# Performance work log

Hardware: AMD Instinct MI355X
Metric: run time of the kernel (lower is better)

The kernel has to match this reference:

```python
import jax, jax.numpy as jnp
import numpy as np

B, T, E, H, R = 1, 2048, 4096, 16, 64
D = E // H
SCALE_ATTN = float(np.sqrt(D))


def _i8_linear(x, W, b, alpha, beta):
    # W8A8B8O8Linear: int8 in, int8 weight/bias, int8 out with requant epilogue
    acc = jnp.einsum('bte,oe->bto', x.astype(jnp.int32), W.astype(jnp.int32)).astype(jnp.float32)
    y = alpha * acc + beta * b.astype(jnp.float32)
    return jnp.clip(jnp.round(y), -128, 127).astype(jnp.int8)


def _rotate_every_two(x):
    x1, x2 = x[..., ::2], x[..., 1::2]
    return jnp.stack([-x2, x1], axis=-1).reshape(x.shape)


def _sincos(seq_len, dim):
    inv_freq = 1.0 / (10000.0 ** (jnp.arange(0, dim, 2, dtype=jnp.float32) / dim))
    ang = jnp.arange(seq_len, dtype=jnp.float32)[:, None] * inv_freq[None, :]
    return jnp.sin(ang), jnp.cos(ang)


def _apply_rotary(x, sin, cos):
    # duplicate_interleave -> repeat each freq twice along last dim
    sin = jnp.repeat(sin, 2, axis=-1)[None, :, None, :]
    cos = jnp.repeat(cos, 2, axis=-1)[None, :, None, :]
    return x * cos + _rotate_every_two(x) * sin


def setup_inputs():
    key = jax.random.key(0)
    ks = jax.random.split(key, 9)
    i8 = lambda k, s: jax.random.randint(k, s, -128, 128, dtype=jnp.int32).astype(jnp.int8)
    return {
        'hidden_states': i8(ks[0], (B, T, E)),
        'Wq': i8(ks[1], (E, E)), 'bq': i8(ks[2], (E,)),
        'Wk': i8(ks[3], (E, E)), 'bk': i8(ks[4], (E,)),
        'Wv': i8(ks[5], (E, E)), 'bv': i8(ks[6], (E,)),
        'Wo': i8(ks[7], (E, E)),
        'b_out': jax.random.normal(ks[8], (E,), dtype=jnp.float32),
        'alpha_q': 2e-4, 'beta_q': 1.0,
        'alpha_k': 2e-4, 'beta_k': 1.0,
        'alpha_v': 2e-4, 'beta_v': 1.0,
        'alpha_qk': 1e-3, 'alpha_pv': 1e-2, 'alpha_out': 2e-4,
    }


def reference(hidden_states, Wq, bq, Wk, bk, Wv, bv, Wo, b_out,
              alpha_q, beta_q, alpha_k, beta_k, alpha_v, beta_v,
              alpha_qk, alpha_pv, alpha_out):
    # int8 q/k/v projections -> [B, T, H, D]
    q = _i8_linear(hidden_states, Wq, bq, alpha_q, beta_q).reshape(B, T, H, D)
    k = _i8_linear(hidden_states, Wk, bk, alpha_k, beta_k).reshape(B, T, H, D)
    v = _i8_linear(hidden_states, Wv, bv, alpha_v, beta_v).reshape(B, T, H, D)
    v = v.transpose(0, 2, 1, 3)  # [B, H, T, D] int8

    # fused rotary on first R dims (float math on dequantized-per-tensor int8 codes)
    sin, cos = _sincos(T, R)
    qf, kf = q.astype(jnp.float32), k.astype(jnp.float32)
    qf = jnp.concatenate([_apply_rotary(qf[..., :R], sin, cos), qf[..., R:]], axis=-1)
    kf = jnp.concatenate([_apply_rotary(kf[..., :R], sin, cos), kf[..., R:]], axis=-1)
    # torch .to(int8) truncates toward zero
    to_i8 = lambda x: jnp.clip(jnp.trunc(x), -128, 127).astype(jnp.int8)
    q = to_i8(qf.transpose(0, 2, 1, 3))  # [B, H, T, D]
    k = to_i8(kf.transpose(0, 2, 1, 3))

    scores = alpha_qk * jnp.einsum('bhtd,bhsd->bhts', q.astype(jnp.int32), k.astype(jnp.int32)).astype(jnp.float32)
    causal = jnp.tril(jnp.ones((T, T), dtype=bool))
    scores = jnp.where(causal, scores, jnp.finfo(jnp.float32).min)
    probs = jax.nn.softmax(scores / SCALE_ATTN, axis=-1)
    probs = jnp.round(probs * 127.0).astype(jnp.int8)  # requant probs to int8

    acc = jnp.einsum('bhts,bhsd->bhtd', probs.astype(jnp.int32), v.astype(jnp.int32)).astype(jnp.float32)
    attn_out = jnp.clip(jnp.round(alpha_pv * acc), -128, 127).astype(jnp.int8)
    attn_out = attn_out.transpose(0, 2, 1, 3).reshape(B, T, E)  # merge heads

    # W8A8BFP32OFP32Linear
    out = alpha_out * jnp.einsum('bte,oe->bto', attn_out.astype(jnp.int32), Wo.astype(jnp.int32)).astype(jnp.float32) + b_out
    return out
```

## Files before the change

kernel.cpp:

```cpp
#include <hip/hip_runtime.h>
#include <cstdint>
#include <cmath>

#define T_ 2048
#define E_ 4096
#define H_ 16
#define D_ 256
#define NF 32

typedef int v4i  __attribute__((ext_vector_type(4)));

__device__ __forceinline__ int dot4(int a, int b, int c) {
#if __has_builtin(__builtin_amdgcn_sdot4)
  return __builtin_amdgcn_sdot4(a, b, c, false);
#else
  c += ((a << 24) >> 24) * ((b << 24) >> 24);
  c += ((a << 16) >> 24) * ((b << 16) >> 24);
  c += ((a <<  8) >> 24) * ((b <<  8) >> 24);
  c += (a >> 24) * (b >> 24);
  return c;
#endif
}

__device__ __forceinline__ int pack4i(int4 v) {
  return (v.x & 255) | ((v.y & 255) << 8) | ((v.z & 255) << 16) | (v.w << 24);
}

#define GLD_LDS16(g, l)                                                        \
  __builtin_amdgcn_global_load_lds(                                            \
      (const __attribute__((address_space(1))) void*)(g),                      \
      (__attribute__((address_space(3))) void*)(l), 16, 0, 0)

__global__ void sincos_kernel(float* __restrict__ sinT, float* __restrict__ cosT) {
  int idx = blockIdx.x * 256 + threadIdx.x;
  int t = idx >> 5, j = idx & 31;
  float invf = (float)exp(-(double)j * (log(10000.0) / 32.0));
  float ang = (float)t * invf;
  sinT[idx] = (float)sin((double)ang);
  cosT[idx] = (float)cos((double)ang);
}

__global__ __launch_bounds__(256) void repack5_kernel(
    const int* __restrict__ sx, const int* __restrict__ s1,
    const int* __restrict__ s2, const int* __restrict__ s3,
    const int* __restrict__ s4,
    int8_t* __restrict__ dx, int8_t* __restrict__ d1,
    int8_t* __restrict__ d2, int8_t* __restrict__ d3,
    int8_t* __restrict__ d4) {
  const int w = blockIdx.y;
  if (w == 0 && blockIdx.x >= (T_ * E_ / 16) / 256) return;
  const int* __restrict__ src =
      (w == 0) ? sx : (w == 1 ? s1 : (w == 2 ? s2 : (w == 3 ? s3 : s4)));
  int8_t* __restrict__ dst =
      (w == 0) ? dx : (w == 1 ? d1 : (w == 2 ? d2 : (w == 3 ? d3 : d4)));
  size_t i = (size_t)blockIdx.x * 256 + threadIdx.x;
  const int4* s = (const int4*)src + i * 4;
  int4 a = s[0], b = s[1], c = s[2], d = s[3];
  int4 o;
  o.x = pack4i(a); o.y = pack4i(b); o.z = pack4i(c); o.w = pack4i(d);
  ((int4*)dst)[i] = o;
}

__global__ __launch_bounds__(256, 2) void qkv_fused_mfma(
    const int8_t* __restrict__ x8,
    const int8_t* __restrict__ Wq8, const int* __restrict__ bq,
    const int8_t* __restrict__ Wk8, const int* __restrict__ bk,
    const int8_t* __restrict__ Wv8, const int* __restrict__ bv,
    const float* __restrict__ alpq, const float* __restrict__ betq,
    const float* __restrict__ alpk, const float* __restrict__ betk,
    const float* __restrict__ alpv, const float* __restrict__ betv,
    const float* __restrict__ sinT, const float* __restrict__ cosT,
    int8_t* __restrict__ Q8, int8_t* __restrict__ K8, int8_t* __restrict__ VT)
{
  __shared__ int8_t As[2][8192];
  __shared__ int8_t Bs[2][3][8192];

  const int tid  = threadIdx.x;
  const int wave = tid >> 6, lane = tid & 63;
  const int wm = wave >> 1, wn = wave & 1;
  const int t0 = blockIdx.x * 128, o0 = blockIdx.y * 128;

  const int srow = lane >> 2;
  const int scol = ((lane & 3) ^ ((lane >> 3) & 3)) * 16;
  const int col  = lane & 15;
  const int quad = lane >> 4;

  v4i accQ[4][4] = {}, accK[4][4] = {}, accV[4][4] = {};

  const int8_t* gA0 = x8  + (size_t)(t0 + wave * 32 + srow) * E_ + scol;
  const int8_t* gBq = Wq8 + (size_t)(o0 + wave * 32 + srow) * E_ + scol;
  const int8_t* gBk = Wk8 + (size_t)(o0 + wave * 32 + srow) * E_ + scol;
  const int8_t* gBv = Wv8 + (size_t)(o0 + wave * 32 + srow) * E_ + scol;

#define STAGE_F(bufi, kt) do {                                                 \
    const int e0_ = (kt) * 64;                                                 \
    GLD_LDS16(gA0 + e0_,           As[bufi] + wave * 2048);                    \
    GLD_LDS16(gA0 + e0_ + 16 * E_, As[bufi] + wave * 2048 + 1024);             \
    GLD_LDS16(gBq + e0_,           Bs[bufi][0] + wave * 2048);                 \
    GLD_LDS16(gBq + e0_ + 16 * E_, Bs[bufi][0] + wave * 2048 + 1024);          \
    GLD_LDS16(gBk + e0_,           Bs[bufi][1] + wave * 2048);                 \
    GLD_LDS16(gBk + e0_ + 16 * E_, Bs[bufi][1] + wave * 2048 + 1024);          \
    GLD_LDS16(gBv + e0_,           Bs[bufi][2] + wave * 2048);                 \
    GLD_LDS16(gBv + e0_ + 16 * E_, Bs[bufi][2] + wave * 2048 + 1024);          \
  } while (0)

  int aoff[4], boff[4];
  #pragma unroll
  for (int i = 0; i < 4; ++i) {
    const int ra = wm * 64 + i * 16 + col;
    aoff[i] = ra * 64 + ((quad ^ ((ra >> 1) & 3)) * 16);
    const int rb = wn * 64 + i * 16 + col;
    boff[i] = rb * 64 + ((quad ^ ((rb >> 1) & 3)) * 16);
  }

  STAGE_F(0, 0);
  STAGE_F(1, 1);

  for (int kt = 0; kt < 64; ++kt) {
    const int cur = kt & 1;
    if (kt == 63) asm volatile("s_waitcnt vmcnt(0)" ::: "memory");
    else          asm volatile("s_waitcnt vmcnt(8)" ::: "memory");
    __builtin_amdgcn_s_barrier();
    v4i a[4];
    #pragma unroll
    for (int i = 0; i < 4; ++i)
      a[i] = *(const v4i*)(As[cur] + aoff[i]);
    __builtin_amdgcn_s_setprio(1);
    {
      v4i b[4];
      #pragma unroll
      for (int j = 0; j < 4; ++j) b[j] = *(const v4i*)(Bs[cur][0] + boff[j]);
      #pragma unroll
      for (int i = 0; i < 4; ++i)
        #pragma unroll
        for (int j = 0; j < 4; ++j)
          accQ[i][j] = __builtin_amdgcn_mfma_i32_16x16x64_i8(a[i], b[j], accQ[i][j], 0, 0, 0);
      #pragma unroll
      for (int j = 0; j < 4; ++j) b[j] = *(const v4i*)(Bs[cur][1] + boff[j]);
      #pragma unroll
      for (int i = 0; i < 4; ++i)
        #pragma unroll
        for (int j = 0; j < 4; ++j)
          accK[i][j] = __builtin_amdgcn_mfma_i32_16x16x64_i8(a[i], b[j], accK[i][j], 0, 0, 0);
      #pragma unroll
      for (int j = 0; j < 4; ++j) b[j] = *(const v4i*)(Bs[cur][2] + boff[j]);
      #pragma unroll
      for (int i = 0; i < 4; ++i)
        #pragma unroll
        for (int j = 0; j < 4; ++j)
          accV[i][j] = __builtin_amdgcn_mfma_i32_16x16x64_i8(a[i], b[j], accV[i][j], 0, 0, 0);
    }
    __builtin_amdgcn_s_setprio(0);
    __builtin_amdgcn_s_barrier();
    if (kt + 2 < 64) STAGE_F(cur, kt + 2);
  }
#undef STAGE_F

  const bool ropeWave = ((o0 & 128) == 0) && (wn == 0);
  #pragma unroll
  for (int m = 0; m < 3; ++m) {
    const int* __restrict__ bsp = (m == 0) ? bq : (m == 1 ? bk : bv);
    const float alpha = (m == 0) ? alpq[0] : (m == 1 ? alpk[0] : alpv[0]);
    const float beta  = (m == 0) ? betq[0] : (m == 1 ? betk[0] : betv[0]);
    int8_t* __restrict__ dst = (m == 0) ? Q8 : (m == 1 ? K8 : VT);
    #pragma unroll
    for (int j = 0; j < 4; ++j) {
      const int o  = o0 + wn * 64 + j * 16 + col;
      const int h  = o >> 8;
      const int dd = o & 255;
      const float bb = (float)bsp[o];
      const int jj = dd >> 1;
      #pragma unroll
      for (int i = 0; i < 4; ++i) {
        const int tb = t0 + wm * 64 + i * 16 + quad * 4;
        int qb[4];
        #pragma unroll
        for (int r = 0; r < 4; ++r) {
          float v = __fadd_rn(__fmul_rn(alpha, (float)(m == 0 ? accQ[i][j][r]
                                         : (m == 1 ? accK[i][j][r] : accV[i][j][r]))),
                              __fmul_rn(beta, bb));
          v = rintf(v);
          v = fminf(fmaxf(v, -128.0f), 127.0f);
          qb[r] = (int)v;
        }
        if (m < 2 && ropeWave) {
          #pragma unroll
          for (int r = 0; r < 4; ++r) {
            float y  = (float)qb[r];
            float yo = __shfl_xor(y, 1);
            const int t = tb + r;
            const float s = sinT[t * NF + jj];
            const float c = cosT[t * NF + jj];
            float rv = ((col & 1) == 0)
                ? __fadd_rn(__fmul_rn(y, c), __fmul_rn(-yo, s))
                : __fadd_rn(__fmul_rn(y, c), __fmul_rn(yo, s));
            qb[r] = (int)fminf(fmaxf(truncf(rv), -128.0f), 127.0f);
          }
        }
        if (m == 2) {
          int packed = (qb[0] & 255) | ((qb[1] & 255) << 8) |
                       ((qb[2] & 255) << 16) | ((qb[3] & 255) << 24);
          *(int*)(dst + ((size_t)h * 256 + dd) * T_ + tb) = packed;
        } else {
          #pragma unroll
          for (int r = 0; r < 4; ++r)
            dst[((size_t)h * T_ + tb + r) * D_ + dd] = (int8_t)qb[r];
        }
      }
    }
  }
}

__global__ __launch_bounds__(256, 3) void out_gemm_mfma(
    const int8_t* __restrict__ xa, const int8_t* __restrict__ Wo8,
    const float* __restrict__ b_out, const float* __restrict__ p_aout,
    float* __restrict__ out)
{
  const float alpha = p_aout[0];
  __shared__ int8_t As[3][8192];
  __shared__ int8_t Bs[3][8192];

  const int tid  = threadIdx.x;
  const int wave = tid >> 6, lane = tid & 63;
  const int wm = wave >> 1, wn = wave & 1;
  const int t0 = blockIdx.x * 128, o0 = blockIdx.y * 128;
  const int srow = lane >> 2;
  const int scol = ((lane & 3) ^ ((lane >> 3) & 3)) * 16;
  const int col = lane & 15, quad = lane >> 4;

  v4i acc[4][4] = {};
  const int8_t* gA0 = xa  + (size_t)(t0 + wave * 32 + srow) * E_ + scol;
  const int8_t* gB0 = Wo8 + (size_t)(o0 + wave * 32 + srow) * E_ + scol;

#define STAGE_OUT(bufi, kt) do {                                               \
    const int e0_ = (kt) * 64;                                                 \
    GLD_LDS16(gA0 + e0_,           As[bufi] + wave * 2048);                    \
    GLD_LDS16(gA0 + e0_ + 16 * E_, As[bufi] + wave * 2048 + 1024);             \
    GLD_LDS16(gB0 + e0_,           Bs[bufi] + wave * 2048);                    \
    GLD_LDS16(gB0 + e0_ + 16 * E_, Bs[bufi] + wave * 2048 + 1024);             \
  } while (0)

  int aoff[4], boff[4];
  #pragma unroll
  for (int i = 0; i < 4; ++i) {
    const int ra = wm * 64 + i * 16 + col;
    aoff[i] = ra * 64 + ((quad ^ ((ra >> 1) & 3)) * 16);
    const int rb = wn * 64 + i * 16 + col;
    boff[i] = rb * 64 + ((quad ^ ((rb >> 1) & 3)) * 16);
  }

  STAGE_OUT(0, 0);
  STAGE_OUT(1, 1);

  int cur = 0;
  for (int kt = 0; kt < 64; ++kt) {
    if (kt == 63) asm volatile("s_waitcnt vmcnt(0)" ::: "memory");
    else          asm volatile("s_waitcnt vmcnt(4)" ::: "memory");
    __builtin_amdgcn_s_barrier();
    if (kt < 62) {
      int nb = cur + 2; if (nb >= 3) nb -= 3;
      STAGE_OUT(nb, kt + 2);
    }
    v4i a[4], b[4];
    #pragma unroll
    for (int i = 0; i < 4; ++i)
      a[i] = *(const v4i*)(As[cur] + aoff[i]);
    #pragma unroll
    for (int j = 0; j < 4; ++j)
      b[j] = *(const v4i*)(Bs[cur] + boff[j]);
    __builtin_amdgcn_s_setprio(1);
    #pragma unroll
    for (int i = 0; i < 4; ++i)
      #pragma unroll
      for (int j = 0; j < 4; ++j)
        acc[i][j] = __builtin_amdgcn_mfma_i32_16x16x64_i8(a[i], b[j], acc[i][j], 0, 0, 0);
    __builtin_amdgcn_s_setprio(0);
    cur = (cur == 2) ? 0 : cur + 1;
  }
#undef STAGE_OUT

  #pragma unroll
  for (int j = 0; j < 4; ++j) {
    const int o = o0 + wn * 64 + j * 16 + col;
    const float bb = b_out[o];
    #pragma unroll
    for (int i = 0; i < 4; ++i) {
      #pragma unroll
      for (int r = 0; r < 4; ++r) {
        const int t = t0 + wm * 64 + i * 16 + quad * 4 + r;
        out[(size_t)t * E_ + o] = __fadd_rn(__fmul_rn(alpha, (float)acc[i][j][r]), bb);
      }
    }
  }
}

__global__ __launch_bounds__(256) void attn_ms_chunk(
    const int8_t* __restrict__ Q8, const int8_t* __restrict__ K8,
    const float* __restrict__ p_aqk,
    float* __restrict__ mPart, float* __restrict__ sPart)
{
  const int ch = blockIdx.x;
  const int qi = blockIdx.y;
  const int h  = blockIdx.z;
  if ((ch << 2) > qi) return;

  __shared__ int8_t Qs[4 * 4096];
  __shared__ int8_t KVs[16384];
  __shared__ float  mred[64][2];
  __shared__ float  sred[64][2];

  const int t0  = qi * 64;
  const int tid = threadIdx.x;
  const int wave = tid >> 6, lane = tid & 63;
  const int wm = wave >> 1, wn = wave & 1;
  const int col = lane & 15, quad = lane >> 4;
  const int srow = lane >> 2, scol = (lane & 3) * 16;
  const float aqk = p_aqk[0] * 0.0625f;

  {
    const int8_t* g = Q8 + ((size_t)h * T_ + t0 + wave * 16 + srow) * D_ + scol;
    #pragma unroll
    for (int c = 0; c < 4; ++c)
      GLD_LDS16(g + c * 64, Qs + c * 4096 + wave * 1024);
  }

  const int it0 = ch * 4;
  const int it1 = (it0 + 3 < qi) ? (it0 + 3) : qi;

  float m[8], sm[8];
  #pragma unroll
  for (int u = 0; u < 8; ++u) { m[u] = -INFINITY; sm[u] = 0.0f; }

  for (int it = it0; it <= it1; ++it) {
    const int s0 = it * 64;
    __syncthreads();
    {
      const int8_t* g = K8 + ((size_t)h * T_ + s0 + wave * 16 + srow) * D_ + scol;
      #pragma unroll
      for (int c = 0; c < 4; ++c)
        GLD_LDS16(g + c * 64, KVs + c * 4096 + wave * 1024);
    }
    __syncthreads();
    v4i accS[2][2] = {};
    #pragma unroll
    for (int c = 0; c < 4; ++c) {
      v4i a[2], b[2];
      #pragma unroll
      for (int i = 0; i < 2; ++i)
        a[i] = *(const v4i*)(Qs + c * 4096 + (wm * 32 + i * 16 + col) * 64 + quad * 16);
      #pragma unroll
      for (int j = 0; j < 2; ++j)
        b[j] = *(const v4i*)(KVs + c * 4096 + (wn * 32 + j * 16 + col) * 64 + quad * 16);
      #pragma unroll
      for (int i = 0; i < 2; ++i)
        #pragma unroll
        for (int j = 0; j < 2; ++j)
          accS[i][j] = __builtin_amdgcn_mfma_i32_16x16x64_i8(a[i], b[j], accS[i][j], 0, 0, 0);
    }
    const bool diag = (s0 == t0);
    #pragma unroll
    for (int i = 0; i < 2; ++i) {
      #pragma unroll
      for (int r = 0; r < 4; ++r) {
        const int ri = i * 4 + r;
        const int qrow = t0 + wm * 32 + i * 16 + quad * 4 + r;
        #pragma unroll
        for (int j = 0; j < 2; ++j) {
          const int s = s0 + wn * 32 + j * 16 + col;
          if (!diag || s <= qrow) {
            float l = __fmul_rn(aqk, (float)accS[i][j][r]);
            if (l > m[ri]) { sm[ri] = sm[ri] * expf(m[ri] - l) + 1.0f; m[ri] = l; }
            else           { sm[ri] += expf(l - m[ri]); }
          }
        }
      }
    }
  }

  #pragma unroll
  for (int u = 0; u < 8; ++u) {
    #pragma unroll
    for (int off = 1; off < 16; off <<= 1) {
      float om = __shfl_xor(m[u], off);
      float os = __shfl_xor(sm[u], off);
      float mm = fmaxf(m[u], om);
      float e1 = (m[u] == mm) ? 1.0f : expf(m[u] - mm);
      float e2 = (om   == mm) ? 1.0f : expf(om - mm);
      sm[u] = sm[u] * e1 + os * e2;
      m[u] = mm;
    }
  }
  __syncthreads();
  if (col == 0) {
    #pragma unroll
    for (int u = 0; u < 8; ++u) {
      int row = wm * 32 + (u >> 2) * 16 + quad * 4 + (u & 3);
      mred[row][wn] = m[u];
      sred[row][wn] = sm[u];
    }
  }
  __syncthreads();
  if (col == 0 && wn == 0) {
    #pragma unroll
    for (int u = 0; u < 8; ++u) {
      int row = wm * 32 + (u >> 2) * 16 + quad * 4 + (u & 3);
      float m0 = mred[row][0], m1 = mred[row][1];
      float sa = sred[row][0], sb = sred[row][1];
      float mm = fmaxf(m0, m1);
      float e0 = (m0 == mm) ? 1.0f : expf(m0 - mm);
      float e1 = (m1 == mm) ? 1.0f : expf(m1 - mm);
      size_t base = (((size_t)h * 32 + qi) * 64 + row) * 8 + ch;
      mPart[base] = mm;
      sPart[base] = __fadd_rn(__fmul_rn(sa, e0), __fmul_rn(sb, e1));
    }
  }
}

__global__ __launch_bounds__(256) void attn_pv_chunk(
    const int8_t* __restrict__ Q8, const int8_t* __restrict__ K8,
    const int8_t* __restrict__ VT,
    const float* __restrict__ p_aqk,
    const float* __restrict__ mPart, const float* __restrict__ sPart,
    int* __restrict__ P0, int* __restrict__ P1)
{
  const int cc = blockIdx.x;
  const int qi = 31 - blockIdx.y;
  const int h  = blockIdx.z;
  if (cc == 1 && qi < 16) return;

  __shared__ int8_t Qs[4 * 4096];
  __shared__ int8_t KVs[16384];
  __shared__ int8_t Ps[64][64];

  const int t0  = qi * 64;
  const int tid = threadIdx.x;
  const int wave = tid >> 6, lane = tid & 63;
  const int wm = wave >> 1, wn = wave & 1;
  const int col = lane & 15, quad = lane >> 4;
  const int srow = lane >> 2, scol = (lane & 3) * 16;
  const float aqk = p_aqk[0] * 0.0625f;

  {
    const int8_t* g = Q8 + ((size_t)h * T_ + t0 + wave * 16 + srow) * D_ + scol;
    #pragma unroll
    for (int c = 0; c < 4; ++c)
      GLD_LDS16(g + c * 64, Qs + c * 4096 + wave * 1024);
  }

  float mF[8], sF[8];
  const int nch = (qi >> 2) + 1;
  #pragma unroll
  for (int u = 0; u < 8; ++u) {
    const int row = wm * 32 + (u >> 2) * 16 + quad * 4 + (u & 3);
    const float* mp = mPart + (((size_t)h * 32 + qi) * 64 + row) * 8;
    const float* sp = sPart + (((size_t)h * 32 + qi) * 64 + row) * 8;
    float m = mp[0], s = sp[0];
    for (int c = 1; c < nch; ++c) {
      float mc = mp[c], sc = sp[c];
      float mm = fmaxf(m, mc);
      float e1 = (m  == mm) ? 1.0f : expf(m - mm);
      float e2 = (mc == mm) ? 1.0f : expf(mc - mm);
      s = __fadd_rn(__fmul_rn(s, e1), __fmul_rn(sc, e2));
      m = mm;
    }
    mF[u] = m;
    sF[u] = s;
  }

  const int it0 = cc * 16;
  const int it1 = (it0 + 15 < qi) ? (it0 + 15) : qi;

  v4i pv[2][8] = {};
  for (int it = it0; it <= it1; ++it) {
    const int s0 = it * 64;
    __syncthreads();
    {
      const int8_t* g = K8 + ((size_t)h * T_ + s0 + wave * 16 + srow) * D_ + scol;
      #pragma unroll
      for (int c = 0; c < 4; ++c)
        GLD_LDS16(g + c * 64, KVs + c * 4096 + wave * 1024);
    }
    __syncthreads();
    v4i accS[2][2] = {};
    #pragma unroll
    for (int c = 0; c < 4; ++c) {
      v4i a[2], b[2];
      #pragma unroll
      for (int i = 0; i < 2; ++i)
        a[i] = *(const v4i*)(Qs + c * 4096 + (wm * 32 + i * 16 + col) * 64 + quad * 16);
      #pragma unroll
      for (int j = 0; j < 2; ++j)
        b[j] = *(const v4i*)(KVs + c * 4096 + (wn * 32 + j * 16 + col) * 64 + quad * 16);
      #pragma unroll
      for (int i = 0; i < 2; ++i)
        #pragma unroll
        for (int j = 0; j < 2; ++j)
          accS[i][j] = __builtin_amdgcn_mfma_i32_16x16x64_i8(a[i], b[j], accS[i][j], 0, 0, 0);
    }
    __syncthreads();
    {
      #pragma unroll
      for (int c = 0; c < 4; ++c) {
        const int drow = (wave * 4 + c) * 16 + srow;
        GLD_LDS16(VT + ((size_t)h * 256 + drow) * T_ + s0 + scol,
                  KVs + (wave * 4 + c) * 1024);
      }
    }
    const bool diag = (s0 == t0);
    #pragma unroll
    for (int i = 0; i < 2; ++i) {
      #pragma unroll
      for (int r = 0; r < 4; ++r) {
        const int ri = i * 4 + r;
        const int qrow = t0 + wm * 32 + i * 16 + quad * 4 + r;
        #pragma unroll
        for (int j = 0; j < 2; ++j) {
          const int s = s0 + wn * 32 + j * 16 + col;
          int q = 0;
          if (!diag || s <= qrow) {
            float l = __fmul_rn(aqk, (float)accS[i][j][r]);
            float p = expf(l - mF[ri]) / sF[ri];
            q = (int)rintf(__fmul_rn(p, 127.0f));
          }
          Ps[wm * 32 + i * 16 + quad * 4 + r][wn * 32 + j * 16 + col] = (int8_t)q;
        }
      }
    }
    __syncthreads();
    v4i a2[2], b2[8];
    #pragma unroll
    for (int i = 0; i < 2; ++i)
      a2[i] = *(const v4i*)&Ps[wm * 32 + i * 16 + col][quad * 16];
    #pragma unroll
    for (int dt = 0; dt < 8; ++dt)
      b2[dt] = *(const v4i*)(KVs + (wn * 128 + dt * 16 + col) * 64 + quad * 16);
    #pragma unroll
    for (int i = 0; i < 2; ++i)
      #pragma unroll
      for (int dt = 0; dt < 8; ++dt)
        pv[i][dt] = __builtin_amdgcn_mfma_i32_16x16x64_i8(a2[i], b2[dt], pv[i][dt], 0, 0, 0);
  }

  int* __restrict__ dst = (cc == 0)
      ? P0 + (((size_t)h * 32 + qi) << 14)
      : P1 + (((size_t)h * 16 + (qi - 16)) << 14);
  #pragma unroll
  for (int i = 0; i < 2; ++i) {
    #pragma unroll
    for (int r = 0; r < 4; ++r) {
      const int trow = wm * 32 + i * 16 + quad * 4 + r;
      #pragma unroll
      for (int dt = 0; dt < 8; ++dt) {
        const int d = wn * 128 + dt * 16 + col;
        dst[trow * 256 + d] = pv[i][dt][r];
      }
    }
  }
}

__global__ __launch_bounds__(256) void attn_pv_combine(
    const int* __restrict__ P0, const int* __restrict__ P1,
    const float* __restrict__ p_apv, int8_t* __restrict__ attn8)
{
  const float apv = p_apv[0];
  int idx = blockIdx.x * 256 + threadIdx.x;
  int d4  = idx & 63;
  int row = (idx >> 6) & 63;
  int qi  = (idx >> 12) & 31;
  int h   = idx >> 17;
  size_t off = (((size_t)h * 32 + qi) << 14) + row * 256 + d4 * 4;
  int4 a = *(const int4*)(P0 + off);
  if (qi >= 16) {
    size_t off1 = (((size_t)h * 16 + (qi - 16)) << 14) + row * 256 + d4 * 4;
    int4 b1 = *(const int4*)(P1 + off1);
    a.x += b1.x; a.y += b1.y; a.z += b1.z; a.w += b1.w;
  }
  int q[4];
  int vv[4] = {a.x, a.y, a.z, a.w};
  #pragma unroll
  for (int r = 0; r < 4; ++r) {
    float y = rintf(__fmul_rn(apv, (float)vv[r]));
    y = fminf(fmaxf(y, -128.0f), 127.0f);
    q[r] = (int)y;
  }
  int packed = (q[0] & 255) | ((q[1] & 255) << 8) | ((q[2] & 255) << 16) | ((q[3] & 255) << 24);
  int t = qi * 64 + row;
  *(int*)(attn8 + (size_t)t * E_ + h * D_ + d4 * 4) = packed;
}

__global__ __launch_bounds__(256) void attn_mfma(
    const int8_t* __restrict__ Q8, const int8_t* __restrict__ K8,
    const int8_t* __restrict__ VT,
    const float* __restrict__ p_aqk, const float* __restrict__ p_apv,
    int8_t* __restrict__ attn8)
{
  __shared__ int8_t Qs[4 * 4096];
  __shared__ int8_t KVs[16384];
  __shared__ int8_t Ps[64][64];
  __shared__ float  mred[64][2];
  __shared__ float  sred[64][2];

  const int h   = blockIdx.y;
  const int t0  = blockIdx.x * 64;
  const int tid = threadIdx.x;
  const int wave = tid >> 6, lane = tid & 63;
  const int wm = wave >> 1, wn = wave & 1;
  const int col = lane & 15, quad = lane >> 4;
  const int srow = lane >> 2, scol = (lane & 3) * 16;
  const float aqk = p_aqk[0] * 0.0625f;
  const float apv = p_apv[0];

  {
    const int8_t* g = Q8 + ((size_t)h * T_ + t0 + wave * 16 + srow) * D_ + scol;
    #pragma unroll
    for (int c = 0; c < 4; ++c)
      GLD_LDS16(g + c * 64, Qs + c * 4096 + wave * 1024);
  }

  const int nt = t0 / 64 + 1;

  float m[8], sm[8];
  #pragma unroll
  for (int u = 0; u < 8; ++u) { m[u] = -INFINITY; sm[u] = 0.0f; }

  for (int it = 0; it < nt; ++it) {
    const int s0 = it * 64;
    __syncthreads();
    {
      const int8_t* g = K8 + ((size_t)h * T_ + s0 + wave * 16 + srow) * D_ + scol;
      #pragma unroll
      for (int c = 0; c < 4; ++c)
        GLD_LDS16(g + c * 64, KVs + c * 4096 + wave * 1024);
    }
    __syncthreads();
    v4i accS[2][2] = {};
    #pragma unroll
    for (int c = 0; c < 4; ++c) {
      v4i a[2], b[2];
      #pragma unroll
      for (int i = 0; i < 2; ++i)
        a[i] = *(const v4i*)(Qs + c * 4096 + (wm * 32 + i * 16 + col) * 64 + quad * 16);
      #pragma unroll
      for (int j = 0; j < 2; ++j)
        b[j] = *(const v4i*)(KVs + c * 4096 + (wn * 32 + j * 16 + col) * 64 + quad * 16);
      #pragma unroll
      for (int i = 0; i < 2; ++i)
        #pragma unroll
        for (int j = 0; j < 2; ++j)
          accS[i][j] = __builtin_amdgcn_mfma_i32_16x16x64_i8(a[i], b[j], accS[i][j], 0, 0, 0);
    }
    const bool diag = (s0 == t0);
    #pragma unroll
    for (int i = 0; i < 2; ++i) {
      #pragma unroll
      for (int r = 0; r < 4; ++r) {
        const int ri = i * 4 + r;
        const int qrow = t0 + wm * 32 + i * 16 + quad * 4 + r;
        #pragma unroll
        for (int j = 0; j < 2; ++j) {
          const int s = s0 + wn * 32 + j * 16 + col;
          if (!diag || s <= qrow) {
            float l = __fmul_rn(aqk, (float)accS[i][j][r]);
            if (l > m[ri]) { sm[ri] = sm[ri] * expf(m[ri] - l) + 1.0f; m[ri] = l; }
            else           { sm[ri] += expf(l - m[ri]); }
          }
        }
      }
    }
  }

  #pragma unroll
  for (int u = 0; u < 8; ++u) {
    #pragma unroll
    for (int off = 1; off < 16; off <<= 1) {
      float om = __shfl_xor(m[u], off);
      float os = __shfl_xor(sm[u], off);
      float mm = fmaxf(m[u], om);
      float e1 = (m[u] == mm) ? 1.0f : expf(m[u] - mm);
      float e2 = (om   == mm) ? 1.0f : expf(om - mm);
      sm[u] = sm[u] * e1 + os * e2;
      m[u] = mm;
    }
  }
  __syncthreads();
  if (col == 0) {
    #pragma unroll
    for (int u = 0; u < 8; ++u) {
      int row = wm * 32 + (u >> 2) * 16 + quad * 4 + (u & 3);
      mred[row][wn] = m[u];
      sred[row][wn] = sm[u];
    }
  }
  __syncthreads();
  float mF[8], sF[8];
  #pragma unroll
  for (int u = 0; u < 8; ++u) {
    int row = wm * 32 + (u >> 2) * 16 + quad * 4 + (u & 3);
    float m0 = mred[row][0], m1 = mred[row][1];
    float sa = sred[row][0], sb = sred[row][1];
    float mm = fmaxf(m0, m1);
    float e0 = (m0 == mm) ? 1.0f : expf(m0 - mm);
    float e1 = (m1 == mm) ? 1.0f : expf(m1 - mm);
    mF[u] = mm;
    sF[u] = __fadd_rn(__fmul_rn(sa, e0), __fmul_rn(sb, e1));
  }

  v4i pv[2][8] = {};
  for (int it = 0; it < nt; ++it) {
    const int s0 = it * 64;
    __syncthreads();
    {
      const int8_t* g = K8 + ((size_t)h * T_ + s0 + wave * 16 + srow) * D_ + scol;
      #pragma unroll
      for (int c = 0; c < 4; ++c)
        GLD_LDS16(g + c * 64, KVs + c * 4096 + wave * 1024);
    }
    __syncthreads();
    v4i accS[2][2] = {};
    #pragma unroll
    for (int c = 0; c < 4; ++c) {
      v4i a[2], b[2];
      #pragma unroll
      for (int i = 0; i < 2; ++i)
        a[i] = *(const v4i*)(Qs + c * 4096 + (wm * 32 + i * 16 + col) * 64 + quad * 16);
      #pragma unroll
      for (int j = 0; j < 2; ++j)
        b[j] = *(const v4i*)(KVs + c * 4096 + (wn * 32 + j * 16 + col) * 64 + quad * 16);
      #pragma unroll
      for (int i = 0; i < 2; ++i)
        #pragma unroll
        for (int j = 0; j < 2; ++j)
          accS[i][j] = __builtin_amdgcn_mfma_i32_16x16x64_i8(a[i], b[j], accS[i][j], 0, 0, 0);
    }
    __syncthreads();
    {
      #pragma unroll
      for (int c = 0; c < 4; ++c) {
        const int drow = (wave * 4 + c) * 16 + srow;
        GLD_LDS16(VT + ((size_t)h * 256 + drow) * T_ + s0 + scol,
                  KVs + (wave * 4 + c) * 1024);
      }
    }
    const bool diag = (s0 == t0);
    #pragma unroll
    for (int i = 0; i < 2; ++i) {
      #pragma unroll
      for (int r = 0; r < 4; ++r) {
        const int ri = i * 4 + r;
        const int qrow = t0 + wm * 32 + i * 16 + quad * 4 + r;
        #pragma unroll
        for (int j = 0; j < 2; ++j) {
          const int s = s0 + wn * 32 + j * 16 + col;
          int q = 0;
          if (!diag || s <= qrow) {
            float l = __fmul_rn(aqk, (float)accS[i][j][r]);
            float p = expf(l - mF[ri]) / sF[ri];
            q = (int)rintf(__fmul_rn(p, 127.0f));
          }
          Ps[wm * 32 + i * 16 + quad * 4 + r][wn * 32 + j * 16 + col] = (int8_t)q;
        }
      }
    }
    __syncthreads();
    v4i a2[2], b2[8];
    #pragma unroll
    for (int i = 0; i < 2; ++i)
      a2[i] = *(const v4i*)&Ps[wm * 32 + i * 16 + col][quad * 16];
    #pragma unroll
    for (int dt = 0; dt < 8; ++dt)
      b2[dt] = *(const v4i*)(KVs + (wn * 128 + dt * 16 + col) * 64 + quad * 16);
    #pragma unroll
    for (int i = 0; i < 2; ++i)
      #pragma unroll
      for (int dt = 0; dt < 8; ++dt)
        pv[i][dt] = __builtin_amdgcn_mfma_i32_16x16x64_i8(a2[i], b2[dt], pv[i][dt], 0, 0, 0);
  }

  #pragma unroll
  for (int i = 0; i < 2; ++i) {
    #pragma unroll
    for (int r = 0; r < 4; ++r) {
      const int t = t0 + wm * 32 + i * 16 + quad * 4 + r;
      #pragma unroll
      for (int dt = 0; dt < 8; ++dt) {
        const int d = wn * 128 + dt * 16 + col;
        float y = rintf(__fmul_rn(apv, (float)pv[i][dt][r]));
        y = fminf(fmaxf(y, -128.0f), 127.0f);
        attn8[(size_t)t * E_ + h * D_ + d] = (int8_t)(int)y;
      }
    }
  }
}

__global__ __launch_bounds__(256) void qkv_gemm_fb(
    const int* __restrict__ xp,
    const int* __restrict__ Wqp, const int* __restrict__ bq,
    const int* __restrict__ Wkp, const int* __restrict__ bk,
    const int* __restrict__ Wvp, const int* __restrict__ bv,
    const float* __restrict__ alpq, const float* __restrict__ betq,
    const float* __restrict__ alpk, const float* __restrict__ betk,
    const float* __restrict__ alpv, const float* __restrict__ betv,
    const float* __restrict__ sinT, const float* __restrict__ cosT,
    int8_t* __restrict__ Q8, int8_t* __restrict__ K8, int8_t* __restrict__ VT)
{
  const int mode = blockIdx.z;
  const int* __restrict__ Wp = (mode == 0) ? Wqp : (mode == 1 ? Wkp : Wvp);
  const int* __restrict__ bs = (mode == 0) ? bq  : (mode == 1 ? bk  : bv);
  const float alpha = (mode == 0) ? alpq[0] : (mode == 1 ? alpk[0] : alpv[0]);
  const float beta  = (mode == 0) ? betq[0] : (mode == 1 ? betk[0] : betv[0]);

  __shared__ int As[64 * 17];
  __shared__ int Bs[64 * 17];
  const int tid = threadIdx.x;
  const int tx = tid & 15, ty = tid >> 4;
  const int t0 = blockIdx.x * 64, o0 = blockIdx.y * 64;
  const int lrow = tid >> 2, lc = tid & 3;
  int acc[4][4] = {};

  for (int e0 = 0; e0 < E_; e0 += 64) {
    const int* xr = xp + (size_t)(t0 + lrow) * E_ + e0 + lc * 16;
    const int* wr = Wp + (size_t)(o0 + lrow) * E_ + e0 + lc * 16;
    int a4[4], b4[4];
    #pragma unroll
    for (int u = 0; u < 4; ++u) a4[u] = pack4i(((const int4*)xr)[u]);
    #pragma unroll
    for (int u = 0; u < 4; ++u) b4[u] = pack4i(((const int4*)wr)[u]);
    __syncthreads();
    int* ap = &As[lrow * 17 + lc * 4];
    ap[0] = a4[0]; ap[1] = a4[1]; ap[2] = a4[2]; ap[3] = a4[3];
    int* bp = &Bs[lrow * 17 + lc * 4];
    bp[0] = b4[0]; bp[1] = b4[1]; bp[2] = b4[2]; bp[3] = b4[3];
    __syncthreads();
    #pragma unroll
    for (int kk = 0; kk < 16; ++kk) {
      int a[4], b[4];
      #pragma unroll
      for (int i = 0; i < 4; ++i) a[i] = As[(ty * 4 + i) * 17 + kk];
      #pragma unroll
      for (int j = 0; j < 4; ++j) b[j] = Bs[(tx * 4 + j) * 17 + kk];
      #pragma unroll
      for (int i = 0; i < 4; ++i)
        #pragma unroll
        for (int j = 0; j < 4; ++j)
          acc[i][j] = dot4(a[i], b[j], acc[i][j]);
    }
  }

  const int ob = o0 + tx * 4;
  const int h  = ob >> 8;
  const int dd = ob & 255;
  #pragma unroll
  for (int i = 0; i < 4; ++i) {
    const int t = t0 + ty * 4 + i;
    float y[4];
    #pragma unroll
    for (int j = 0; j < 4; ++j) {
      float v = __fadd_rn(__fmul_rn(alpha, (float)acc[i][j]),
                          __fmul_rn(beta, (float)bs[ob + j]));
      v = rintf(v);
      y[j] = fminf(fmaxf(v, -128.0f), 127.0f);
    }
    int q0, q1, q2, q3;
    if (mode < 2 && dd < 64) {
      const int j0 = dd >> 1;
      const float s0 = sinT[t * NF + j0],     c0 = cosT[t * NF + j0];
      const float s1 = sinT[t * NF + j0 + 1], c1 = cosT[t * NF + j0 + 1];
      float r0 = __fadd_rn(__fmul_rn(y[0], c0), __fmul_rn(-y[1], s0));
      float r1 = __fadd_rn(__fmul_rn(y[1], c0), __fmul_rn( y[0], s0));
      float r2 = __fadd_rn(__fmul_rn(y[2], c1), __fmul_rn(-y[3], s1));
      float r3 = __fadd_rn(__fmul_rn(y[3], c1), __fmul_rn( y[2], s1));
      q0 = (int)fminf(fmaxf(truncf(r0), -128.0f), 127.0f);
      q1 = (int)fminf(fmaxf(truncf(r1), -128.0f), 127.0f);
      q2 = (int)fminf(fmaxf(truncf(r2), -128.0f), 127.0f);
      q3 = (int)fminf(fmaxf(truncf(r3), -128.0f), 127.0f);
    } else {
      q0 = (int)y[0]; q1 = (int)y[1]; q2 = (int)y[2]; q3 = (int)y[3];
    }
    if (mode == 2) {
      VT[((size_t)h * 256 + dd + 0) * T_ + t] = (int8_t)q0;
      VT[((size_t)h * 256 + dd + 1) * T_ + t] = (int8_t)q1;
      VT[((size_t)h * 256 + dd + 2) * T_ + t] = (int8_t)q2;
      VT[((size_t)h * 256 + dd + 3) * T_ + t] = (int8_t)q3;
    } else {
      int8_t* dst = (mode == 0) ? Q8 : K8;
      int packed = (q0 & 255) | ((q1 & 255) << 8) | ((q2 & 255) << 16) | ((q3 & 255) << 24);
      *(int*)(dst + ((size_t)h * T_ + t) * D_ + dd) = packed;
    }
  }
}

__global__ __launch_bounds__(256) void out_gemm_fb(
    const int8_t* __restrict__ xa, const int* __restrict__ Wop,
    const float* __restrict__ b_out, const float* __restrict__ p_aout,
    float* __restrict__ out)
{
  __shared__ int As[64 * 17];
  __shared__ int Bs[64 * 17];
  const float alpha = p_aout[0];
  const int tid = threadIdx.x;
  const int tx = tid & 15, ty = tid >> 4;
  const int t0 = blockIdx.x * 64, o0 = blockIdx.y * 64;
  const int lrow = tid >> 2, lc = tid & 3;
  int acc[4][4] = {};

  for (int e0 = 0; e0 < E_; e0 += 64) {
    int4 av4 = *(const int4*)(xa + (size_t)(t0 + lrow) * E_ + e0 + lc * 16);
    const int* wr = Wop + (size_t)(o0 + lrow) * E_ + e0 + lc * 16;
    int b4[4];
    #pragma unroll
    for (int u = 0; u < 4; ++u) b4[u] = pack4i(((const int4*)wr)[u]);
    __syncthreads();
    int* ap = &As[lrow * 17 + lc * 4];
    ap[0] = av4.x; ap[1] = av4.y; ap[2] = av4.z; ap[3] = av4.w;
    int* bp = &Bs[lrow * 17 + lc * 4];
    bp[0] = b4[0]; bp[1] = b4[1]; bp[2] = b4[2]; bp[3] = b4[3];
    __syncthreads();
    #pragma unroll
    for (int kk = 0; kk < 16; ++kk) {
      int a[4], b[4];
      #pragma unroll
      for (int i = 0; i < 4; ++i) a[i] = As[(ty * 4 + i) * 17 + kk];
      #pragma unroll
      for (int j = 0; j < 4; ++j) b[j] = Bs[(tx * 4 + j) * 17 + kk];
      #pragma unroll
      for (int i = 0; i < 4; ++i)
        #pragma unroll
        for (int j = 0; j < 4; ++j)
          acc[i][j] = dot4(a[i], b[j], acc[i][j]);
    }
  }
  #pragma unroll
  for (int i = 0; i < 4; ++i) {
    const int t = t0 + ty * 4 + i;
    const int ob = o0 + tx * 4;
    #pragma unroll
    for (int j = 0; j < 4; ++j) {
      out[(size_t)t * E_ + ob + j] =
          __fadd_rn(__fmul_rn(alpha, (float)acc[i][j]), b_out[ob + j]);
    }
  }
}

extern "C" void kernel_launch(void* const* d_in, const int* in_sizes, int n_in,
                              void* d_out, int out_size, void* d_ws, size_t ws_size,
                              hipStream_t stream) {
  const int* hs   = (const int*)d_in[0];
  const int* Wq   = (const int*)d_in[1];
  const int* bq   = (const int*)d_in[2];
  const int* Wk   = (const int*)d_in[3];
  const int* bk   = (const int*)d_in[4];
  const int* Wv   = (const int*)d_in[5];
  const int* bv   = (const int*)d_in[6];
  const int* Wo   = (const int*)d_in[7];
  const float* b_out = (const float*)d_in[8];
  const float* aq   = (const float*)d_in[9];
  const float* btq  = (const float*)d_in[10];
  const float* ak   = (const float*)d_in[11];
  const float* btk  = (const float*)d_in[12];
  const float* av   = (const float*)d_in[13];
  const float* btv  = (const float*)d_in[14];
  const float* aqk  = (const float*)d_in[15];
  const float* apv  = (const float*)d_in[16];
  const float* aout = (const float*)d_in[17];

  const size_t SEG = (size_t)H_ * T_ * D_;
  char* ws = (char*)d_ws;
  int8_t* Q8    = (int8_t*)ws;
  int8_t* K8    = Q8 + SEG;
  int8_t* VT    = K8 + SEG;
  int8_t* attn8 = VT + SEG;
  int8_t* x8    = attn8;
  float*  sinT  = (float*)(ws + 4 * SEG);
  float*  cosT  = sinT + T_ * NF;
  int8_t* Wq8   = (int8_t*)(cosT + T_ * NF);
  int8_t* Wk8   = Wq8 + (size_t)E_ * E_;
  int8_t* Wv8   = Wk8 + (size_t)E_ * E_;
  int8_t* Wo8   = Wv8 + (size_t)E_ * E_;
  const size_t NEED = 4 * SEG + 2 * (size_t)T_ * NF * 4 + 4 * (size_t)E_ * E_;
  const bool big = (ws_size >= NEED);

  sincos_kernel<<<(T_ * NF) / 256, 256, 0, stream>>>(sinT, cosT);

  if (big) {
    repack5_kernel<<<dim3((E_ * E_ / 16) / 256, 5), 256, 0, stream>>>(
        hs, Wq, Wk, Wv, Wo, x8, Wq8, Wk8, Wv8, Wo8);
    qkv_fused_mfma<<<dim3(T_ / 128, E_ / 128), 256, 0, stream>>>(
        x8, Wq8, bq, Wk8, bk, Wv8, bv, aq, btq, ak, btk, av, btv,
        sinT, cosT, Q8, K8, VT);

    int*   P1g   = (int*)Wq8;
    int*   P0g   = (int*)Wk8;
    float* mPart = (float*)attn8;
    float* sPart = mPart + (size_t)H_ * 32 * 64 * 8;

    attn_ms_chunk<<<dim3(8, 32, H_), 256, 0, stream>>>(Q8, K8, aqk, mPart, sPart);
    attn_pv_chunk<<<dim3(2, 32, H_), 256, 0, stream>>>(
        Q8, K8, VT, aqk, mPart, sPart, P0g, P1g);
    attn_pv_combine<<<(H_ * 32 * 64 * 64) / 256, 256, 0, stream>>>(
        P0g, P1g, apv, attn8);

    out_gemm_mfma<<<dim3(T_ / 128, E_ / 128), 256, 0, stream>>>(
        attn8, Wo8, b_out, aout, (float*)d_out);
  } else {
    qkv_gemm_fb<<<dim3(T_ / 64, E_ / 64, 3), 256, 0, stream>>>(
        hs, Wq, bq, Wk, bk, Wv, bv, aq, btq, ak, btk, av, btv,
        sinT, cosT, Q8, K8, VT);
    attn_mfma<<<dim3(T_ / 64, H_), 256, 0, stream>>>(Q8, K8, VT, aqk, apv, attn8);
    out_gemm_fb<<<dim3(T_ / 64, E_ / 64), 256, 0, stream>>>(
        attn8, Wo, b_out, aout, (float*)d_out);
  }
}
```

Before: 704.6 us.

## Split QKV GEMM per projection with triple buffering; prefetch K tiles in attention

The fused QKV kernel, which held three 64-register accumulator sets, becomes one GEMM per projection selected by blockIdx.z. It uses a 3-stage LDS ring that issues the next load right after a single barrier, and launch bounds are raised to 3 blocks per CU. The attention kernels now double-buffer K tiles in LDS with swizzled offsets, and PV reads V operands straight from global memory into registers instead of staging them through LDS. The aim is higher occupancy and overlap of memory with MFMA, at the cost of re-reading x from memory three times and relying on uncoalesced direct V loads.

```diff
diff --git a/kernel.cpp b/kernel.cpp
--- a/kernel.cpp
+++ b/kernel.cpp
@@ -61,7 +61,7 @@
   ((int4*)dst)[i] = o;
 }
 
-__global__ __launch_bounds__(256, 2) void qkv_fused_mfma(
+__global__ __launch_bounds__(256, 3) void qkv_gemm_mfma(
     const int8_t* __restrict__ x8,
     const int8_t* __restrict__ Wq8, const int* __restrict__ bq,
     const int8_t* __restrict__ Wk8, const int* __restrict__ bk,
@@ -72,8 +72,14 @@
     const float* __restrict__ sinT, const float* __restrict__ cosT,
     int8_t* __restrict__ Q8, int8_t* __restrict__ K8, int8_t* __restrict__ VT)
 {
-  __shared__ int8_t As[2][8192];
-  __shared__ int8_t Bs[2][3][8192];
+  const int mode = blockIdx.z;
+  const int8_t* __restrict__ W = (mode == 0) ? Wq8 : (mode == 1 ? Wk8 : Wv8);
+  const int* __restrict__ bs   = (mode == 0) ? bq  : (mode == 1 ? bk  : bv);
+  const float alpha = (mode == 0) ? alpq[0] : (mode == 1 ? alpk[0] : alpv[0]);
+  const float beta  = (mode == 0) ? betq[0] : (mode == 1 ? betk[0] : betv[0]);
+
+  __shared__ int8_t As[3][8192];
+  __shared__ int8_t Bs[3][8192];
 
   const int tid  = threadIdx.x;
   const int wave = tid >> 6, lane = tid & 63;
@@ -85,23 +91,17 @@
   const int col  = lane & 15;
   const int quad = lane >> 4;
 
-  v4i accQ[4][4] = {}, accK[4][4] = {}, accV[4][4] = {};
-
-  const int8_t* gA0 = x8  + (size_t)(t0 + wave * 32 + srow) * E_ + scol;
-  const int8_t* gBq = Wq8 + (size_t)(o0 + wave * 32 + srow) * E_ + scol;
-  const int8_t* gBk = Wk8 + (size_t)(o0 + wave * 32 + srow) * E_ + scol;
-  const int8_t* gBv = Wv8 + (size_t)(o0 + wave * 32 + srow) * E_ + scol;
-
-#define STAGE_F(bufi, kt) do {                                                 \
+  v4i acc[4][4] = {};
+
+  const int8_t* gA0 = x8 + (size_t)(t0 + wave * 32 + srow) * E_ + scol;
+  const int8_t* gB0 = W  + (size_t)(o0 + wave * 32 + srow) * E_ + scol;
+
+#define STAGE_QKV(bufi, kt) do {                                               \
     const int e0_ = (kt) * 64;                                                 \
     GLD_LDS16(gA0 + e0_,           As[bufi] + wave * 2048);                    \
     GLD_LDS16(gA0 + e0_ + 16 * E_, As[bufi] + wave * 2048 + 1024);             \
-    GLD_LDS16(gBq + e0_,           Bs[bufi][0] + wave * 2048);                 \
-    GLD_LDS16(gBq + e0_ + 16 * E_, Bs[bufi][0] + wave * 2048 + 1024);          \
-    GLD_LDS16(gBk + e0_,           Bs[bufi][1] + wave * 2048);                 \
-    GLD_LDS16(gBk + e0_ + 16 * E_, Bs[bufi][1] + wave * 2048 + 1024);          \
-    GLD_LDS16(gBv + e0_,           Bs[bufi][2] + wave * 2048);                 \
-    GLD_LDS16(gBv + e0_ + 16 * E_, Bs[bufi][2] + wave * 2048 + 1024);          \
+    GLD_LDS16(gB0 + e0_,           Bs[bufi] + wave * 2048);                    \
+    GLD_LDS16(gB0 + e0_ + 16 * E_, Bs[bufi] + wave * 2048 + 1024);             \
   } while (0)
 
   int aoff[4], boff[4];
@@ -113,99 +113,79 @@
     boff[i] = rb * 64 + ((quad ^ ((rb >> 1) & 3)) * 16);
   }
 
-  STAGE_F(0, 0);
-  STAGE_F(1, 1);
-
+  STAGE_QKV(0, 0);
+  STAGE_QKV(1, 1);
+
+  int cur = 0;
   for (int kt = 0; kt < 64; ++kt) {
-    const int cur = kt & 1;
     if (kt == 63) asm volatile("s_waitcnt vmcnt(0)" ::: "memory");
-    else          asm volatile("s_waitcnt vmcnt(8)" ::: "memory");
+    else          asm volatile("s_waitcnt vmcnt(4)" ::: "memory");
     __builtin_amdgcn_s_barrier();
-    v4i a[4];
+    if (kt < 62) {
+      int nb = cur + 2; if (nb >= 3) nb -= 3;
+      STAGE_QKV(nb, kt + 2);
+    }
+    v4i a[4], b[4];
     #pragma unroll
     for (int i = 0; i < 4; ++i)
       a[i] = *(const v4i*)(As[cur] + aoff[i]);
+    #pragma unroll
+    for (int j = 0; j < 4; ++j)
+      b[j] = *(const v4i*)(Bs[cur] + boff[j]);
     __builtin_amdgcn_s_setprio(1);
-    {
-      v4i b[4];
-      #pragma unroll
-      for (int j = 0; j < 4; ++j) b[j] = *(const v4i*)(Bs[cur][0] + boff[j]);
-      #pragma unroll
-      for (int i = 0; i < 4; ++i)
-        #pragma unroll
-        for (int j = 0; j < 4; ++j)
-          accQ[i][j] = __builtin_amdgcn_mfma_i32_16x16x64_i8(a[i], b[j], accQ[i][j], 0, 0, 0);
-      #pragma unroll
-      for (int j = 0; j < 4; ++j) b[j] = *(const v4i*)(Bs[cur][1] + boff[j]);
-      #pragma unroll
-      for (int i = 0; i < 4; ++i)
-        #pragma unroll
-        for (int j = 0; j < 4; ++j)
-          accK[i][j] = __builtin_amdgcn_mfma_i32_16x16x64_i8(a[i], b[j], accK[i][j], 0, 0, 0);
-      #pragma unroll
-      for (int j = 0; j < 4; ++j) b[j] = *(const v4i*)(Bs[cur][2] + boff[j]);
-      #pragma unroll
-      for (int i = 0; i < 4; ++i)
-        #pragma unroll
-        for (int j = 0; j < 4; ++j)
-          accV[i][j] = __builtin_amdgcn_mfma_i32_16x16x64_i8(a[i], b[j], accV[i][j], 0, 0, 0);
-    }
+    #pragma unroll
+    for (int i = 0; i < 4; ++i)
+      #pragma unroll
+      for (int j = 0; j < 4; ++j)
+        acc[i][j] = __builtin_amdgcn_mfma_i32_16x16x64_i8(a[i], b[j], acc[i][j], 0, 0, 0);
     __builtin_amdgcn_s_setprio(0);
-    __builtin_amdgcn_s_barrier();
-    if (kt + 2 < 64) STAGE_F(cur, kt + 2);
-  }
-#undef STAGE_F
-
-  const bool ropeWave = ((o0 & 128) == 0) && (wn == 0);
-  #pragma unroll
-  for (int m = 0; m < 3; ++m) {
-    const int* __restrict__ bsp = (m == 0) ? bq : (m == 1 ? bk : bv);
-    const float alpha = (m == 0) ? alpq[0] : (m == 1 ? alpk[0] : alpv[0]);
-    const float beta  = (m == 0) ? betq[0] : (m == 1 ? betk[0] : betv[0]);
-    int8_t* __restrict__ dst = (m == 0) ? Q8 : (m == 1 ? K8 : VT);
-    #pragma unroll
-    for (int j = 0; j < 4; ++j) {
-      const int o  = o0 + wn * 64 + j * 16 + col;
-      const int h  = o >> 8;
-      const int dd = o & 255;
-      const float bb = (float)bsp[o];
-      const int jj = dd >> 1;
-      #pragma unroll
-      for (int i = 0; i < 4; ++i) {
-        const int tb = t0 + wm * 64 + i * 16 + quad * 4;
-        int qb[4];
+    cur = (cur == 2) ? 0 : cur + 1;
+  }
+#undef STAGE_QKV
+
+  int8_t* __restrict__ dst = (mode == 0) ? Q8 : (mode == 1 ? K8 : VT);
+  const bool ropeWave = (mode < 2) && ((o0 & 128) == 0) && (wn == 0);
+  #pragma unroll
+  for (int j = 0; j < 4; ++j) {
+    const int o  = o0 + wn * 64 + j * 16 + col;
+    const int h  = o >> 8;
+    const int dd = o & 255;
+    const float bb = (float)bs[o];
+    const int jj = dd >> 1;
+    #pragma unroll
+    for (int i = 0; i < 4; ++i) {
+      const int tb = t0 + wm * 64 + i * 16 + quad * 4;
+      int qb[4];
+      #pragma unroll
+      for (int r = 0; r < 4; ++r) {
+        float v = __fadd_rn(__fmul_rn(alpha, (float)acc[i][j][r]),
+                            __fmul_rn(beta, bb));
+        v = rintf(v);
+        v = fminf(fmaxf(v, -128.0f), 127.0f);
+        qb[r] = (int)v;
+      }
+      if (ropeWave) {
         #pragma unroll
         for (int r = 0; r < 4; ++r) {
-          float v = __fadd_rn(__fmul_rn(alpha, (float)(m == 0 ? accQ[i][j][r]
-                                         : (m == 1 ? accK[i][j][r] : accV[i][j][r]))),
-                              __fmul_rn(beta, bb));
-          v = rintf(v);
-          v = fminf(fmaxf(v, -128.0f), 127.0f);
-          qb[r] = (int)v;
+          float y  = (float)qb[r];
+          float yo = __shfl_xor(y, 1);
+          const int t = tb + r;
+          const float s = sinT[t * NF + jj];
+          const float c = cosT[t * NF + jj];
+          float rv = ((col & 1) == 0)
+              ? __fadd_rn(__fmul_rn(y, c), __fmul_rn(-yo, s))
+              : __fadd_rn(__fmul_rn(y, c), __fmul_rn(yo, s));
+          qb[r] = (int)fminf(fmaxf(truncf(rv), -128.0f), 127.0f);
         }
-        if (m < 2 && ropeWave) {
-          #pragma unroll
-          for (int r = 0; r < 4; ++r) {
-            float y  = (float)qb[r];
-            float yo = __shfl_xor(y, 1);
-            const int t = tb + r;
-            const float s = sinT[t * NF + jj];
-            const float c = cosT[t * NF + jj];
-            float rv = ((col & 1) == 0)
-                ? __fadd_rn(__fmul_rn(y, c), __fmul_rn(-yo, s))
-                : __fadd_rn(__fmul_rn(y, c), __fmul_rn(yo, s));
-            qb[r] = (int)fminf(fmaxf(truncf(rv), -128.0f), 127.0f);
-          }
-        }
-        if (m == 2) {
-          int packed = (qb[0] & 255) | ((qb[1] & 255) << 8) |
-                       ((qb[2] & 255) << 16) | ((qb[3] & 255) << 24);
-          *(int*)(dst + ((size_t)h * 256 + dd) * T_ + tb) = packed;
-        } else {
-          #pragma unroll
-          for (int r = 0; r < 4; ++r)
-            dst[((size_t)h * T_ + tb + r) * D_ + dd] = (int8_t)qb[r];
-        }
+      }
+      if (mode == 2) {
+        int packed = (qb[0] & 255) | ((qb[1] & 255) << 8) |
+                     ((qb[2] & 255) << 16) | ((qb[3] & 255) << 24);
+        *(int*)(dst + ((size_t)h * 256 + dd) * T_ + tb) = packed;
+      } else {
+        #pragma unroll
+        for (int r = 0; r < 4; ++r)
+          dst[((size_t)h * T_ + tb + r) * D_ + dd] = (int8_t)qb[r];
       }
     }
   }
@@ -305,7 +285,7 @@
   if ((ch << 2) > qi) return;
 
   __shared__ int8_t Qs[4 * 4096];
-  __shared__ int8_t KVs[16384];
+  __shared__ int8_t Ks[2][16384];
   __shared__ float  mred[64][2];
   __shared__ float  sred[64][2];
 
@@ -314,43 +294,58 @@
   const int wave = tid >> 6, lane = tid & 63;
   const int wm = wave >> 1, wn = wave & 1;
   const int col = lane & 15, quad = lane >> 4;
-  const int srow = lane >> 2, scol = (lane & 3) * 16;
+  const int srow = lane >> 2;
+  const int scol = ((lane & 3) ^ ((lane >> 3) & 3)) * 16;
   const float aqk = p_aqk[0] * 0.0625f;
+
+  const int it0 = ch * 4;
+  const int it1 = (it0 + 3 < qi) ? (it0 + 3) : qi;
 
   {
     const int8_t* g = Q8 + ((size_t)h * T_ + t0 + wave * 16 + srow) * D_ + scol;
     #pragma unroll
     for (int c = 0; c < 4; ++c)
       GLD_LDS16(g + c * 64, Qs + c * 4096 + wave * 1024);
-  }
-
-  const int it0 = ch * 4;
-  const int it1 = (it0 + 3 < qi) ? (it0 + 3) : qi;
+    const int8_t* gk = K8 + ((size_t)h * T_ + it0 * 64 + wave * 16 + srow) * D_ + scol;
+    #pragma unroll
+    for (int c = 0; c < 4; ++c)
+      GLD_LDS16(gk + c * 64, Ks[0] + c * 4096 + wave * 1024);
+  }
+  asm volatile("s_waitcnt vmcnt(0)" ::: "memory");
+  __builtin_amdgcn_s_barrier();
+
+  int qoff[2], koff[2];
+  #pragma unroll
+  for (int i = 0; i < 2; ++i) {
+    const int ra = wm * 32 + i * 16 + col;
+    qoff[i] = ra * 64 + ((quad ^ ((ra >> 1) & 3)) * 16);
+    const int rb = wn * 32 + i * 16 + col;
+    koff[i] = rb * 64 + ((quad ^ ((rb >> 1) & 3)) * 16);
+  }
 
   float m[8], sm[8];
   #pragma unroll
   for (int u = 0; u < 8; ++u) { m[u] = -INFINITY; sm[u] = 0.0f; }
 
+  int cur = 0;
   for (int it = it0; it <= it1; ++it) {
     const int s0 = it * 64;
-    __syncthreads();
-    {
-      const int8_t* g = K8 + ((size_t)h * T_ + s0 + wave * 16 + srow) * D_ + scol;
+    if (it < it1) {
+      const int8_t* g = K8 + ((size_t)h * T_ + (it + 1) * 64 + wave * 16 + srow) * D_ + scol;
       #pragma unroll
       for (int c = 0; c < 4; ++c)
-        GLD_LDS16(g + c * 64, KVs + c * 4096 + wave * 1024);
-    }
-    __syncthreads();
+        GLD_LDS16(g + c * 64, Ks[cur ^ 1] + c * 4096 + wave * 1024);
+    }
     v4i accS[2][2] = {};
     #pragma unroll
     for (int c = 0; c < 4; ++c) {
       v4i a[2], b[2];
       #pragma unroll
       for (int i = 0; i < 2; ++i)
-        a[i] = *(const v4i*)(Qs + c * 4096 + (wm * 32 + i * 16 + col) * 64 + quad * 16);
+        a[i] = *(const v4i*)(Qs + c * 4096 + qoff[i]);
       #pragma unroll
       for (int j = 0; j < 2; ++j)
-        b[j] = *(const v4i*)(KVs + c * 4096 + (wn * 32 + j * 16 + col) * 64 + quad * 16);
+        b[j] = *(const v4i*)(Ks[cur] + c * 4096 + koff[j]);
       #pragma unroll
       for (int i = 0; i < 2; ++i)
         #pragma unroll
@@ -375,6 +370,9 @@
         }
       }
     }
+    asm volatile("s_waitcnt vmcnt(0)" ::: "memory");
+    __builtin_amdgcn_s_barrier();
+    cur ^= 1;
   }
 
   #pragma unroll
@@ -429,22 +427,30 @@
   if (cc == 1 && qi < 16) return;
 
   __shared__ int8_t Qs[4 * 4096];
-  __shared__ int8_t KVs[16384];
-  __shared__ int8_t Ps[64][64];
+  __shared__ int8_t Ks[2][16384];
+  __shared__ int8_t Ps[64][80];
 
   const int t0  = qi * 64;
   const int tid = threadIdx.x;
   const int wave = tid >> 6, lane = tid & 63;
   const int wm = wave >> 1, wn = wave & 1;
   const int col = lane & 15, quad = lane >> 4;
-  const int srow = lane >> 2, scol = (lane & 3) * 16;
+  const int srow = lane >> 2;
+  const int scol = ((lane & 3) ^ ((lane >> 3) & 3)) * 16;
   const float aqk = p_aqk[0] * 0.0625f;
+
+  const int it0 = cc * 16;
+  const int it1 = (it0 + 15 < qi) ? (it0 + 15) : qi;
 
   {
     const int8_t* g = Q8 + ((size_t)h * T_ + t0 + wave * 16 + srow) * D_ + scol;
     #pragma unroll
     for (int c = 0; c < 4; ++c)
       GLD_LDS16(g + c * 64, Qs + c * 4096 + wave * 1024);
+    const int8_t* gk = K8 + ((size_t)h * T_ + it0 * 64 + wave * 16 + srow) * D_ + scol;
+    #pragma unroll
+    for (int c = 0; c < 4; ++c)
+      GLD_LDS16(gk + c * 64, Ks[0] + c * 4096 + wave * 1024);
   }
 
   float mF[8], sF[8];
@@ -467,44 +473,48 @@
     sF[u] = s;
   }
 
-  const int it0 = cc * 16;
-  const int it1 = (it0 + 15 < qi) ? (it0 + 15) : qi;
+  asm volatile("s_waitcnt vmcnt(0)" ::: "memory");
+  __builtin_amdgcn_s_barrier();
+
+  int qoff[2], koff[2];
+  #pragma unroll
+  for (int i = 0; i < 2; ++i) {
+    const int ra = wm * 32 + i * 16 + col;
+    qoff[i] = ra * 64 + ((quad ^ ((ra >> 1) & 3)) * 16);
+    const int rb = wn * 32 + i * 16 + col;
+    koff[i] = rb * 64 + ((quad ^ ((rb >> 1) & 3)) * 16);
+  }
 
   v4i pv[2][8] = {};
+  int cur = 0;
   for (int it = it0; it <= it1; ++it) {
     const int s0 = it * 64;
-    __syncthreads();
-    {
-      const int8_t* g = K8 + ((size_t)h * T_ + s0 + wave * 16 + srow) * D_ + scol;
+    v4i vb[8];
+    #pragma unroll
+    for (int dt = 0; dt < 8; ++dt)
+      vb[dt] = *(const v4i*)(VT + ((size_t)h * 256 + wn * 128 + dt * 16 + col) * T_
+                             + s0 + quad * 16);
+    if (it < it1) {
+      const int8_t* g = K8 + ((size_t)h * T_ + (it + 1) * 64 + wave * 16 + srow) * D_ + scol;
       #pragma unroll
       for (int c = 0; c < 4; ++c)
-        GLD_LDS16(g + c * 64, KVs + c * 4096 + wave * 1024);
-    }
-    __syncthreads();
+        GLD_LDS16(g + c * 64, Ks[cur ^ 1] + c * 4096 + wave * 1024);
+    }
     v4i accS[2][2] = {};
     #pragma unroll
     for (int c = 0; c < 4; ++c) {
       v4i a[2], b[2];
       #pragma unroll
       for (int i = 0; i < 2; ++i)
-        a[i] = *(const v4i*)(Qs + c * 4096 + (wm * 32 + i * 16 + col) * 64 + quad * 16);
+        a[i] = *(const v4i*)(Qs + c * 4096 + qoff[i]);
       #pragma unroll
       for (int j = 0; j < 2; ++j)
-        b[j] = *(const v4i*)(KVs + c * 4096 + (wn * 32 + j * 16 + col) * 64 + quad * 16);
+        b[j] = *(const v4i*)(Ks[cur] + c * 4096 + koff[j]);
       #pragma unroll
       for (int i = 0; i < 2; ++i)
         #pragma unroll
         for (int j = 0; j < 2; ++j)
           accS[i][j] = __builtin_amdgcn_mfma_i32_16x16x64_i8(a[i], b[j], accS[i][j], 0, 0, 0);
-    }
-    __syncthreads();
-    {
-      #pragma unroll
-      for (int c = 0; c < 4; ++c) {
-        const int drow = (wave * 4 + c) * 16 + srow;
-        GLD_LDS16(VT + ((size_t)h * 256 + drow) * T_ + s0 + scol,
-                  KVs + (wave * 4 + c) * 1024);
-      }
     }
     const bool diag = (s0 == t0);
     #pragma unroll
@@ -526,19 +536,20 @@
         }
       }
     }
-    __syncthreads();
-    v4i a2[2], b2[8];
+    asm volatile("s_waitcnt lgkmcnt(0)" ::: "memory");
+    __builtin_amdgcn_s_barrier();
+    v4i a2[2];
     #pragma unroll
     for (int i = 0; i < 2; ++i)
       a2[i] = *(const v4i*)&Ps[wm * 32 + i * 16 + col][quad * 16];
     #pragma unroll
-    for (int dt = 0; dt < 8; ++dt)
-      b2[dt] = *(const v4i*)(KVs + (wn * 128 + dt * 16 + col) * 64 + quad * 16);
-    #pragma unroll
     for (int i = 0; i < 2; ++i)
       #pragma unroll
       for (int dt = 0; dt < 8; ++dt)
-        pv[i][dt] = __builtin_amdgcn_mfma_i32_16x16x64_i8(a2[i], b2[dt], pv[i][dt], 0, 0, 0);
+        pv[i][dt] = __builtin_amdgcn_mfma_i32_16x16x64_i8(a2[i], vb[dt], pv[i][dt], 0, 0, 0);
+    asm volatile("s_waitcnt vmcnt(0)" ::: "memory");
+    __builtin_amdgcn_s_barrier();
+    cur ^= 1;
   }
 
   int* __restrict__ dst = (cc == 0)
@@ -984,7 +995,7 @@
   if (big) {
     repack5_kernel<<<dim3((E_ * E_ / 16) / 256, 5), 256, 0, stream>>>(
         hs, Wq, Wk, Wv, Wo, x8, Wq8, Wk8, Wv8, Wo8);
-    qkv_fused_mfma<<<dim3(T_ / 128, E_ / 128), 256, 0, stream>>>(
+    qkv_gemm_mfma<<<dim3(T_ / 128, E_ / 128, 3), 256, 0, stream>>>(
         x8, Wq8, bq, Wk8, bk, Wv8, bv, aq, btq, ak, btk, av, btv,
         sinT, cosT, Q8, K8, VT);
 
```

Measured after the change: 737.9 us. 1.05x slower.
